# Optimization experiments

Measured on AMD Instinct MI355X. Metric: run time of the kernel, lower is better.

## Reference

```python
import jax, jax.numpy as jnp
import numpy as np

NUM_HEADS = 16
DIM = 1024
HEAD_DIM = DIM // NUM_HEADS
SCALE = HEAD_DIM ** -0.5


def setup_inputs() -> dict:
    key = jax.random.key(0)
    ks = jax.random.split(key, 6)
    b, n = 2, 1024
    x = jax.random.normal(ks[0], (b, n, DIM), dtype=jnp.float32)
    Wq = jax.random.normal(ks[1], (DIM, DIM), dtype=jnp.float32) * 0.02
    bq = jnp.zeros((DIM,), dtype=jnp.float32)
    Wkv = jax.random.normal(ks[2], (2 * DIM, DIM), dtype=jnp.float32) * 0.02
    bkv = jnp.zeros((2 * DIM,), dtype=jnp.float32)
    Wp = jax.random.normal(ks[3], (DIM, DIM), dtype=jnp.float32) * 0.02
    bp = jnp.zeros((DIM,), dtype=jnp.float32)
    return {"x": x, "Wq": Wq, "bq": bq, "Wkv": Wkv, "bkv": bkv, "Wp": Wp, "bp": bp}


def reference(x, Wq, bq, Wkv, bkv, Wp, bp):
    b, n, c = x.shape
    h, dh = NUM_HEADS, HEAD_DIM
    # self-attention: y = x
    q = (x @ Wq.T + bq).reshape(b, n, h, dh)              # bnhd
    kv = (x @ Wkv.T + bkv).reshape(b, n, 2, h, dh)
    k, v = kv[:, :, 0], kv[:, :, 1]                       # bmhd each
    attn = jnp.einsum('bnhd,bmhd->bnmh', q, k) * SCALE    # bnmh scores
    attn = jax.nn.softmax(attn, axis=2)                   # softmax over m
    out = jnp.einsum('bnmh,bmhd->bnhd', attn, v).reshape(b, n, c)
    out = out @ Wp.T + bp
    return (out, attn)
```

## Files before the change

### kernel.cpp

```cpp
#include <hip/hip_runtime.h>
#include <hip/hip_bf16.h>
#include <stdint.h>


#define NB   2
#define SEQ  1024
#define CDIM 1024
#define NH   16
#define HD   64
#define ROWS (NB*SEQ)
#define ATT_SCALE 0.125f
#define S23  1028

typedef __attribute__((ext_vector_type(8))) short bf16x8;
typedef __attribute__((ext_vector_type(4))) float f32x4;

#define MFMA16(a,b,c) __builtin_amdgcn_mfma_f32_16x16x32_bf16((a),(b),(c),0,0,0)

static __device__ __forceinline__ unsigned short f2bf(float f) {
  uint32_t x = __builtin_bit_cast(uint32_t, f);
  return (unsigned short)((x + 0x7fffu + ((x >> 16) & 1u)) >> 16);
}
static __device__ __forceinline__ float bf2f(unsigned short u) {
  uint32_t x = ((uint32_t)u) << 16;
  return __builtin_bit_cast(float, x);
}

static __device__ __forceinline__ void gl_lds16(const unsigned short* g,
                                                unsigned short* l) {
  __builtin_amdgcn_global_load_lds(
      (const __attribute__((address_space(1))) unsigned int*)g,
      (__attribute__((address_space(3))) unsigned int*)l,
      16, 0, 0);
}

__global__ __launch_bounds__(256) void k_convert(
    const float* __restrict__ x, const float* __restrict__ Wq,
    const float* __restrict__ Wkv, const float* __restrict__ Wp,
    unsigned short* __restrict__ Xhi, unsigned short* __restrict__ Xlo,
    unsigned short* __restrict__ Whi, unsigned short* __restrict__ Wlo)
{
  const int NX = ROWS * CDIM;
  const int NW = 4096 * CDIM;
  int i = blockIdx.x * 256 + threadIdx.x;
  if (i < NX) {
    float f = x[i];
    unsigned short h = f2bf(f);
    Xhi[i] = h; Xlo[i] = f2bf(f - bf2f(h));
  } else if (i < NX + NW) {
    int w = i - NX;
    int j = w >> 10, c = w & 1023;
    float f = (j < 1024) ? Wq[(size_t)j*1024 + c]
            : (j < 3072) ? Wkv[(size_t)(j-1024)*1024 + c]
                         : Wp[(size_t)(j-3072)*1024 + c];
    unsigned short h = f2bf(f);
    Whi[w] = h; Wlo[w] = f2bf(f - bf2f(h));
  }
}

struct EpiQKV {
  const float* bq; const float* bkv;
  unsigned short *Qhi, *Qlo, *Khi, *Klo, *Vthi, *Vtlo;
  __device__ __forceinline__ void operator()(int m, int n, float v) const {
    if (n < 1024) {
      v += bq[n];
      unsigned short h = f2bf(v);
      size_t o = (size_t)m*1024 + n;
      Qhi[o] = h; Qlo[o] = f2bf(v - bf2f(h));
    } else if (n < 2048) {
      v += bkv[n - 1024];
      size_t o = (size_t)m*1024 + (n - 1024);
      unsigned short h = f2bf(v);
      Khi[o] = h; Klo[o] = f2bf(v - bf2f(h));
    } else {
      v += bkv[n - 1024];
      int c = n - 2048;
      int hh = c >> 6, d = c & 63;
      int b = m >> 10, mm = m & 1023;
      size_t o = ((size_t)((b*NH + hh)*HD + d))*SEQ + mm;
      unsigned short h = f2bf(v);
      Vthi[o] = h; Vtlo[o] = f2bf(v - bf2f(h));
    }
  }
};
struct EpiOut {
  const float* bp; float* out;
  __device__ __forceinline__ void operator()(int m, int n, float v) const {
    out[(size_t)m*1024 + n] = v + bp[n];
  }
};

template <int BM, int BN, class Epi>
__device__ __forceinline__ void gemm_core(
    const unsigned short* __restrict__ Ahi, const unsigned short* __restrict__ Alo, int lda,
    const unsigned short* __restrict__ Bhi, const unsigned short* __restrict__ Blo, int ldb,
    int K, const Epi& epi)
{
  constexpr int FM = BM/32, FN = BN/32;
  constexpr int CA = BM/16, CB = BN/16;
  constexpr int TOT = 2*(CA+CB);
  __shared__ unsigned short sAh[BM*32], sAl[BM*32], sBh[BN*32], sBl[BN*32];
  const int tid  = threadIdx.x;
  const int lane = tid & 63, wave = tid >> 6;
  const int wm = wave & 1, wn = wave >> 1;
  const int bn = blockIdx.x * BN, bm = blockIdx.y * BM;
  const int r = lane & 15, q = lane >> 4;
  const int crow = lane >> 2, ccol = (lane & 3) * 8;

  f32x4 acc[FM][FN];
  #pragma unroll
  for (int i = 0; i < FM; i++)
    #pragma unroll
    for (int j = 0; j < FN; j++) {
      acc[i][j][0]=0.f; acc[i][j][1]=0.f; acc[i][j][2]=0.f; acc[i][j][3]=0.f;
    }

  for (int k0 = 0; k0 < K; k0 += 32) {
    #pragma unroll
    for (int t = 0; t < TOT/4; t++) {
      int c = wave + t*4;
      const unsigned short* gb; unsigned short* sb; int rr, grow, ld;
      if (c < CA)            { gb=Ahi; sb=sAh; rr=c;         grow=bm; ld=lda; }
      else if (c < 2*CA)     { gb=Alo; sb=sAl; rr=c-CA;      grow=bm; ld=lda; }
      else if (c < 2*CA+CB)  { gb=Bhi; sb=sBh; rr=c-2*CA;    grow=bn; ld=ldb; }
      else                   { gb=Blo; sb=sBl; rr=c-2*CA-CB; grow=bn; ld=ldb; }
      int row = rr*16 + crow;
      gl_lds16(gb + (size_t)(grow + row)*ld + k0 + ccol, sb + rr*512);
    }
    __syncthreads();
    bf16x8 ah[FM], al[FM], bh[FN], bl[FN];
    #pragma unroll
    for (int i = 0; i < FM; i++) {
      int oa = (wm*(BM/2) + i*16 + r)*32 + q*8;
      ah[i] = *(const bf16x8*)(sAh + oa);
      al[i] = *(const bf16x8*)(sAl + oa);
    }
    #pragma unroll
    for (int j = 0; j < FN; j++) {
      int ob = (wn*(BN/2) + j*16 + r)*32 + q*8;
      bh[j] = *(const bf16x8*)(sBh + ob);
      bl[j] = *(const bf16x8*)(sBl + ob);
    }
    #pragma unroll
    for (int i = 0; i < FM; i++)
      #pragma unroll
      for (int j = 0; j < FN; j++) {
        acc[i][j] = MFMA16(ah[i], bh[j], acc[i][j]);
        acc[i][j] = MFMA16(ah[i], bl[j], acc[i][j]);
        acc[i][j] = MFMA16(al[i], bh[j], acc[i][j]);
      }
    __syncthreads();
  }
  #pragma unroll
  for (int i = 0; i < FM; i++)
    #pragma unroll
    for (int j = 0; j < FN; j++)
      #pragma unroll
      for (int t = 0; t < 4; t++)
        epi(bm + wm*(BM/2) + i*16 + q*4 + t, bn + wn*(BN/2) + j*16 + r, acc[i][j][t]);
}

__global__ __launch_bounds__(256) void k_gemm_qkv(
    const unsigned short* Xhi, const unsigned short* Xlo,
    const unsigned short* Whi, const unsigned short* Wlo,
    const float* bq, const float* bkv,
    unsigned short* Qhi, unsigned short* Qlo,
    unsigned short* Khi, unsigned short* Klo,
    unsigned short* Vthi, unsigned short* Vtlo)
{
  EpiQKV e{bq, bkv, Qhi, Qlo, Khi, Klo, Vthi, Vtlo};
  gemm_core<128,128>(Xhi, Xlo, CDIM, Whi, Wlo, CDIM, CDIM, e);
}

__global__ __launch_bounds__(256) void k_gemm_out(
    const unsigned short* OAhi, const unsigned short* OAlo,
    const unsigned short* Wphi, const unsigned short* Wplo,
    const float* bp, float* out)
{
  EpiOut e{bp, out};
  gemm_core<64,64>(OAhi, OAlo, CDIM, Wphi, Wplo, CDIM, CDIM, e);
}

static __device__ __forceinline__ void stage_q23(
    const unsigned short* Qhi, const unsigned short* Qlo,
    size_t qrow0, int col0, unsigned short* sQ,
    int wave, int drow, int dseg)
{
  if (wave < 4) {
    int p = wave >> 1, t = wave & 1;
    const unsigned short* g = p ? Qlo : Qhi;
    gl_lds16(g + (qrow0 + t*8 + drow)*CDIM + col0 + dseg*8,
             sQ + p*1024 + t*512);
  }
}
static __device__ __forceinline__ void stage_k23(
    const unsigned short* Khi, const unsigned short* Klo,
    size_t krow0, int col0, unsigned short* dstbuf,
    int wave, int drow, int dseg)
{
  #pragma unroll
  for (int u = 0; u < 4; u++) {
    int c = wave*4 + u;
    int p = c >> 4, t = c & 15;
    const unsigned short* g = p ? Klo : Khi;
    gl_lds16(g + (krow0 + t*8 + drow)*CDIM + col0 + dseg*8,
             dstbuf + p*8192 + t*512);
  }
}

__global__ __launch_bounds__(512) void k_logits_softmax(
    const unsigned short* __restrict__ Qhi, const unsigned short* __restrict__ Qlo,
    const unsigned short* __restrict__ Khi, const unsigned short* __restrict__ Klo,
    unsigned short* __restrict__ P)
{
  const int nt = blockIdx.x, hg = blockIdx.y, b = blockIdx.z;
  const int n0 = nt*16;
  __shared__ unsigned short sQ[2*1024];
  __shared__ unsigned short sK[2][2*8192];
  __shared__ float slab[16*S23];
  __shared__ float red[512];
  __shared__ float gmax[16], gscale[16];
  const int tid = threadIdx.x, lane = tid & 63, wave = tid >> 6;
  const int r = lane & 15, q = lane >> 4;
  const int drow = lane >> 3, dseg = (lane & 7) ^ drow;
  const int sw = r & 7;
  const size_t qrow0 = (size_t)b*SEQ + n0;
  const size_t krow0 = (size_t)b*SEQ;

  {
    int col0 = (hg*8)*HD;
    stage_q23(Qhi, Qlo, qrow0, col0, sQ, wave, drow, dseg);
    stage_k23(Khi, Klo, krow0, col0, sK[0], wave, drow, dseg);
  }

  for (int hh = 0; hh < 8; hh++) {
    const int h = hg*8 + hh;
    const int col0 = h*HD;
    __syncthreads();
    bf16x8 qh[2], ql[2];
    #pragma unroll
    for (int ks = 0; ks < 2; ks++) {
      int phys = r*64 + (((ks*4 + q) ^ sw))*8;
      qh[ks] = *(const bf16x8*)(sQ + phys);
      ql[ks] = *(const bf16x8*)(sQ + 1024 + phys);
    }
    for (int c128 = 0; c128 < 8; c128++) {
      unsigned short* cur = sK[c128 & 1];
      if (c128 < 7)
        stage_k23(Khi, Klo, krow0 + (size_t)(c128+1)*128, col0,
                  sK[(c128+1)&1], wave, drow, dseg);
      {
        const int mb = wave*16;
        f32x4 acc; acc[0]=0.f; acc[1]=0.f; acc[2]=0.f; acc[3]=0.f;
        #pragma unroll
        for (int ks = 0; ks < 2; ks++) {
          int phys = (mb + r)*64 + (((ks*4 + q) ^ sw))*8;
          bf16x8 kh = *(const bf16x8*)(cur + phys);
          bf16x8 kl = *(const bf16x8*)(cur + 8192 + phys);
          acc = MFMA16(qh[ks], kh, acc);
          acc = MFMA16(qh[ks], kl, acc);
          acc = MFMA16(ql[ks], kh, acc);
        }
        #pragma unroll
        for (int t = 0; t < 4; t++)
          slab[(q*4+t)*S23 + c128*128 + mb + r] = acc[t] * ATT_SCALE;
      }
      __syncthreads();
    }
    if (hh < 7) {
      int ncol = (h+1)*HD;
      stage_q23(Qhi, Qlo, qrow0, ncol, sQ, wave, drow, dseg);
      stage_k23(Khi, Klo, krow0, ncol, sK[0], wave, drow, dseg);
    }
    const int n = tid >> 5, c = tid & 31;
    float mx = -1e30f;
    #pragma unroll 8
    for (int j = 0; j < 32; j++)
      mx = fmaxf(mx, slab[n*S23 + c + j*32]);
    red[tid] = mx;
    __syncthreads();
    if (tid < 16) {
      float m2 = red[tid*32];
      for (int j = 1; j < 32; j++) m2 = fmaxf(m2, red[tid*32 + j]);
      gmax[tid] = m2;
    }
    __syncthreads();
    const float gm = gmax[n];
    float s = 0.f;
    #pragma unroll 8
    for (int j = 0; j < 32; j++) {
      int idx = n*S23 + c + j*32;
      float p = __expf(slab[idx] - gm);
      slab[idx] = p;
      s += p;
    }
    red[tid] = s;
    __syncthreads();
    if (tid < 16) {
      float s2 = 0.f;
      for (int j = 0; j < 32; j++) s2 += red[tid*32 + j];
      gscale[tid] = 65535.0f / s2;
    }
    __syncthreads();
    const float sc = gscale[n];
    const size_t pb = ((size_t)((b*NH + h)*SEQ) + n0 + n)*SEQ;
    #pragma unroll
    for (int j = 0; j < 4; j++) {
      int m0 = (j*32 + c)*8;
      float4 v0 = *(const float4*)&slab[n*S23 + m0];
      float4 v1 = *(const float4*)&slab[n*S23 + m0 + 4];
      unsigned int u0 = (unsigned)(v0.x*sc + 0.5f) | ((unsigned)(v0.y*sc + 0.5f) << 16);
      unsigned int u1 = (unsigned)(v0.z*sc + 0.5f) | ((unsigned)(v0.w*sc + 0.5f) << 16);
      unsigned int u2 = (unsigned)(v1.x*sc + 0.5f) | ((unsigned)(v1.y*sc + 0.5f) << 16);
      unsigned int u3 = (unsigned)(v1.z*sc + 0.5f) | ((unsigned)(v1.w*sc + 0.5f) << 16);
      *(uint4*)(P + pb + m0) = make_uint4(u0, u1, u2, u3);
    }
  }
}

__global__ __launch_bounds__(256) void k_attn_write(
    const unsigned short* __restrict__ P, float* __restrict__ attn)
{
  int T = blockIdx.x*256 + threadIdx.x;
  int b = T >> 20, rem = T & 1048575;
  int n = rem >> 10, m = rem & 1023;
  const size_t pb = ((size_t)(b*NH)*SEQ + n)*SEQ + m;
  float v[16];
  #pragma unroll
  for (int h = 0; h < 16; h++)
    v[h] = (float)P[pb + (size_t)h*SEQ*SEQ] * (1.0f/65535.0f);
  size_t ob = ((size_t)(b*SEQ + n)*SEQ + m)*16;
  #pragma unroll
  for (int g = 0; g < 4; g++)
    *(float4*)(attn + ob + g*4) = make_float4(v[g*4], v[g*4+1], v[g*4+2], v[g*4+3]);
}

__global__ __launch_bounds__(256) void k_pv(
    const unsigned short* __restrict__ P,
    const unsigned short* __restrict__ Vthi, const unsigned short* __restrict__ Vtlo,
    unsigned short* __restrict__ OAhi, unsigned short* __restrict__ OAlo)
{
  int nt = blockIdx.x, h = blockIdx.y, b = blockIdx.z;
  int n0 = nt * 64;
  __shared__ unsigned short sPa[64*32], sPb[64*32], sVh[64*32], sVl[64*32];
  const int tid = threadIdx.x, lane = tid & 63, wave = tid >> 6;
  const int wm = wave & 1, wn = wave >> 1;
  const int r = lane & 15, q = lane >> 4;
  const int crow = lane >> 2, ccol = (lane & 3) * 8;
  const size_t pbase = ((size_t)(b*NH + h))*SEQ*SEQ;
  const size_t vbase = ((size_t)(b*NH + h))*HD*SEQ;

  f32x4 acc[2][2];
  #pragma unroll
  for (int i = 0; i < 2; i++)
    #pragma unroll
    for (int j = 0; j < 2; j++) {
      acc[i][j][0]=0.f; acc[i][j][1]=0.f; acc[i][j][2]=0.f; acc[i][j][3]=0.f;
    }

  for (int k0 = 0; k0 < SEQ; k0 += 32) {
    #pragma unroll
    for (int t = 0; t < 2; t++) {
      int c = wave + t*4;
      const unsigned short* gb = (c < 4) ? Vthi : Vtlo;
      unsigned short* sb = (c < 4) ? (unsigned short*)sVh : (unsigned short*)sVl;
      int rr = c & 3;
      int row = rr*16 + crow;
      gl_lds16(gb + vbase + (size_t)row*SEQ + k0 + ccol, sb + rr*512);
    }
    {
      int row = tid >> 2, ch = (tid & 3) * 8;
      uint4 v = *(const uint4*)(P + pbase + (size_t)(n0 + row)*SEQ + k0 + ch);
      unsigned int wds[4] = {v.x, v.y, v.z, v.w};
      unsigned int pa[4], pb4[4];
      #pragma unroll
      for (int e = 0; e < 4; e++) {
        unsigned int lo16 = wds[e] & 0xFFFFu;
        unsigned int hi16 = wds[e] >> 16;
        unsigned int a0 = __builtin_bit_cast(uint32_t, (float)(lo16 & 0xFF00u)) >> 16;
        unsigned int b0 = __builtin_bit_cast(uint32_t, (float)(lo16 & 0x00FFu)) >> 16;
        unsigned int a1 = __builtin_bit_cast(uint32_t, (float)(hi16 & 0xFF00u)) >> 16;
        unsigned int b1 = __builtin_bit_cast(uint32_t, (float)(hi16 & 0x00FFu)) >> 16;
        pa[e]  = a0 | (a1 << 16);
        pb4[e] = b0 | (b1 << 16);
      }
      *(uint4*)(sPa + row*32 + ch) = make_uint4(pa[0],pa[1],pa[2],pa[3]);
      *(uint4*)(sPb + row*32 + ch) = make_uint4(pb4[0],pb4[1],pb4[2],pb4[3]);
    }
    __syncthreads();
    bf16x8 pa[2], pb2[2], vh[2], vl[2];
    #pragma unroll
    for (int i = 0; i < 2; i++) {
      int off = (wm*32 + i*16 + r)*32 + q*8;
      pa[i]  = *(const bf16x8*)(sPa + off);
      pb2[i] = *(const bf16x8*)(sPb + off);
    }
    #pragma unroll
    for (int j = 0; j < 2; j++) {
      int off = (wn*32 + j*16 + r)*32 + q*8;
      vh[j] = *(const bf16x8*)(sVh + off);
      vl[j] = *(const bf16x8*)(sVl + off);
    }
    #pragma unroll
    for (int i = 0; i < 2; i++)
      #pragma unroll
      for (int j = 0; j < 2; j++) {
        acc[i][j] = MFMA16(pa[i],  vh[j], acc[i][j]);
        acc[i][j] = MFMA16(pb2[i], vh[j], acc[i][j]);
        acc[i][j] = MFMA16(pa[i],  vl[j], acc[i][j]);
      }
    __syncthreads();
  }
  #pragma unroll
  for (int i = 0; i < 2; i++)
    #pragma unroll
    for (int t = 0; t < 4; t++) {
      int nn = n0 + wm*32 + i*16 + q*4 + t;
      #pragma unroll
      for (int j = 0; j < 2; j++) {
        int d = wn*32 + j*16 + r;
        float val = acc[i][j][t] * (1.0f/65535.0f);
        size_t o = (size_t)(b*SEQ + nn)*CDIM + h*HD + d;
        unsigned short hb = f2bf(val);
        OAhi[o] = hb; OAlo[o] = f2bf(val - bf2f(hb));
      }
    }
}

extern "C" void kernel_launch(void* const* d_in, const int* in_sizes, int n_in,
                              void* d_out, int out_size, void* d_ws, size_t ws_size,
                              hipStream_t stream)
{
  const float* x   = (const float*)d_in[0];
  const float* Wq  = (const float*)d_in[1];
  const float* bq  = (const float*)d_in[2];
  const float* Wkv = (const float*)d_in[3];
  const float* bkv = (const float*)d_in[4];
  const float* Wp  = (const float*)d_in[5];
  const float* bp  = (const float*)d_in[6];

  float* out  = (float*)d_out;
  float* attn = out + (size_t)ROWS*CDIM;

  char* w = (char*)d_ws;
  unsigned short* Xhi  = (unsigned short*)w; w += (size_t)ROWS*CDIM*2;
  unsigned short* Xlo  = (unsigned short*)w; w += (size_t)ROWS*CDIM*2;
  unsigned short* Whi  = (unsigned short*)w; w += (size_t)4096*CDIM*2;
  unsigned short* Wlo  = (unsigned short*)w; w += (size_t)4096*CDIM*2;
  unsigned short* Qhi  = (unsigned short*)w; w += (size_t)ROWS*CDIM*2;
  unsigned short* Qlo  = (unsigned short*)w; w += (size_t)ROWS*CDIM*2;
  unsigned short* Khi  = (unsigned short*)w; w += (size_t)ROWS*CDIM*2;
  unsigned short* Klo  = (unsigned short*)w; w += (size_t)ROWS*CDIM*2;
  unsigned short* Vthi = (unsigned short*)w; w += (size_t)NB*NH*HD*SEQ*2;
  unsigned short* Vtlo = (unsigned short*)w; w += (size_t)NB*NH*HD*SEQ*2;
  unsigned short* OAhi = (unsigned short*)w; w += (size_t)ROWS*CDIM*2;
  unsigned short* OAlo = (unsigned short*)w; w += (size_t)ROWS*CDIM*2;
  unsigned short* P    = (unsigned short*)w; w += (size_t)NB*NH*SEQ*SEQ*2;

  k_convert<<<dim3((ROWS*CDIM + 4096*CDIM)/256), 256, 0, stream>>>(
      x, Wq, Wkv, Wp, Xhi, Xlo, Whi, Wlo);

  k_gemm_qkv<<<dim3(3072/128, 2048/128), 256, 0, stream>>>(
      Xhi, Xlo, Whi, Wlo, bq, bkv, Qhi, Qlo, Khi, Klo, Vthi, Vtlo);

  k_logits_softmax<<<dim3(SEQ/16, 2, NB), 512, 0, stream>>>(
      Qhi, Qlo, Khi, Klo, P);

  k_pv<<<dim3(SEQ/64, NH, NB), 256, 0, stream>>>(P, Vthi, Vtlo, OAhi, OAlo);

  k_gemm_out<<<dim3(1024/64, 2048/64), 256, 0, stream>>>(
      OAhi, OAlo, Whi + (size_t)3072*CDIM, Wlo + (size_t)3072*CDIM, bp, out);

  k_attn_write<<<dim3((NB*SEQ*SEQ)/256), 256, 0, stream>>>(P, attn);
}
```

Measured before the change: 410.0 us.

## Replace LDS softmax slab with two-pass online softmax recomputing logits

The logits/softmax kernel no longer keeps a 16x1024 fp32 score slab in shared memory. It runs a first pass that computes QK^T with an online running max and sum in registers, then a second pass that recomputes the logits and writes normalized P directly. The attention scale moves into the Q projection epilogue, and the grid now covers one head and 32 query rows per block, so far less LDS is used and occupancy can rise. The cost is doing the QK MFMA work twice and reloading the K tiles.

```diff
diff --git a/kernel.cpp b/kernel.cpp
--- a/kernel.cpp
+++ b/kernel.cpp
@@ -10,7 +10,6 @@
 #define HD   64
 #define ROWS (NB*SEQ)
 #define ATT_SCALE 0.125f
-#define S23  1028
 
 typedef __attribute__((ext_vector_type(8))) short bf16x8;
 typedef __attribute__((ext_vector_type(4))) float f32x4;
@@ -63,7 +62,7 @@
   unsigned short *Qhi, *Qlo, *Khi, *Klo, *Vthi, *Vtlo;
   __device__ __forceinline__ void operator()(int m, int n, float v) const {
     if (n < 1024) {
-      v += bq[n];
+      v = (v + bq[n]) * ATT_SCALE;
       unsigned short h = f2bf(v);
       size_t o = (size_t)m*1024 + n;
       Qhi[o] = h; Qlo[o] = f2bf(v - bf2f(h));
@@ -181,45 +180,18 @@
   gemm_core<64,64>(OAhi, OAlo, CDIM, Wphi, Wplo, CDIM, CDIM, e);
 }
 
-static __device__ __forceinline__ void stage_q23(
-    const unsigned short* Qhi, const unsigned short* Qlo,
-    size_t qrow0, int col0, unsigned short* sQ,
-    int wave, int drow, int dseg)
-{
-  if (wave < 4) {
-    int p = wave >> 1, t = wave & 1;
-    const unsigned short* g = p ? Qlo : Qhi;
-    gl_lds16(g + (qrow0 + t*8 + drow)*CDIM + col0 + dseg*8,
-             sQ + p*1024 + t*512);
-  }
-}
-static __device__ __forceinline__ void stage_k23(
-    const unsigned short* Khi, const unsigned short* Klo,
-    size_t krow0, int col0, unsigned short* dstbuf,
-    int wave, int drow, int dseg)
-{
-  #pragma unroll
-  for (int u = 0; u < 4; u++) {
-    int c = wave*4 + u;
-    int p = c >> 4, t = c & 15;
-    const unsigned short* g = p ? Klo : Khi;
-    gl_lds16(g + (krow0 + t*8 + drow)*CDIM + col0 + dseg*8,
-             dstbuf + p*8192 + t*512);
-  }
-}
-
-__global__ __launch_bounds__(512) void k_logits_softmax(
+__global__ __launch_bounds__(512, 4) void k_logits_softmax(
     const unsigned short* __restrict__ Qhi, const unsigned short* __restrict__ Qlo,
     const unsigned short* __restrict__ Khi, const unsigned short* __restrict__ Klo,
     unsigned short* __restrict__ P)
 {
-  const int nt = blockIdx.x, hg = blockIdx.y, b = blockIdx.z;
-  const int n0 = nt*16;
-  __shared__ unsigned short sQ[2*1024];
-  __shared__ unsigned short sK[2][2*8192];
-  __shared__ float slab[16*S23];
-  __shared__ float red[512];
-  __shared__ float gmax[16], gscale[16];
+  const int nt = blockIdx.x, h = blockIdx.y, b = blockIdx.z;
+  const int n0 = nt*32;
+  const int col0 = h*HD;
+  __shared__ unsigned short sQ[2*32*64];
+  __shared__ unsigned short sK[2][2*128*64];
+  __shared__ float redm[8][32], reds[8][32];
+  __shared__ float gm_s[32], sc_s[32];
   const int tid = threadIdx.x, lane = tid & 63, wave = tid >> 6;
   const int r = lane & 15, q = lane >> 4;
   const int drow = lane >> 3, dseg = (lane & 7) ^ drow;
@@ -227,94 +199,126 @@
   const size_t qrow0 = (size_t)b*SEQ + n0;
   const size_t krow0 = (size_t)b*SEQ;
 
+  auto stageK = [&](int c, int buf) {
+    unsigned short* dst = sK[buf];
+    #pragma unroll
+    for (int u = 0; u < 4; u++) {
+      int cc = wave*4 + u;
+      int p = cc >> 4, t = cc & 15;
+      const unsigned short* g = p ? Klo : Khi;
+      gl_lds16(g + (krow0 + (size_t)c*128 + t*8 + drow)*CDIM + col0 + dseg*8,
+               dst + p*8192 + t*512);
+    }
+  };
+
   {
-    int col0 = (hg*8)*HD;
-    stage_q23(Qhi, Qlo, qrow0, col0, sQ, wave, drow, dseg);
-    stage_k23(Khi, Klo, krow0, col0, sK[0], wave, drow, dseg);
-  }
-
-  for (int hh = 0; hh < 8; hh++) {
-    const int h = hg*8 + hh;
-    const int col0 = h*HD;
-    __syncthreads();
-    bf16x8 qh[2], ql[2];
+    int p = wave >> 2, t = wave & 3;
+    const unsigned short* g = p ? Qlo : Qhi;
+    gl_lds16(g + (qrow0 + t*8 + drow)*CDIM + col0 + dseg*8,
+             sQ + p*2048 + t*512);
+    stageK(0, 0);
+  }
+  __syncthreads();
+
+  bf16x8 qh[2][2], ql[2][2];
+  #pragma unroll
+  for (int nf = 0; nf < 2; nf++)
     #pragma unroll
     for (int ks = 0; ks < 2; ks++) {
-      int phys = r*64 + (((ks*4 + q) ^ sw))*8;
-      qh[ks] = *(const bf16x8*)(sQ + phys);
-      ql[ks] = *(const bf16x8*)(sQ + 1024 + phys);
-    }
-    for (int c128 = 0; c128 < 8; c128++) {
-      unsigned short* cur = sK[c128 & 1];
-      if (c128 < 7)
-        stage_k23(Khi, Klo, krow0 + (size_t)(c128+1)*128, col0,
-                  sK[(c128+1)&1], wave, drow, dseg);
-      {
-        const int mb = wave*16;
-        f32x4 acc; acc[0]=0.f; acc[1]=0.f; acc[2]=0.f; acc[3]=0.f;
-        #pragma unroll
-        for (int ks = 0; ks < 2; ks++) {
-          int phys = (mb + r)*64 + (((ks*4 + q) ^ sw))*8;
-          bf16x8 kh = *(const bf16x8*)(cur + phys);
-          bf16x8 kl = *(const bf16x8*)(cur + 8192 + phys);
-          acc = MFMA16(qh[ks], kh, acc);
-          acc = MFMA16(qh[ks], kl, acc);
-          acc = MFMA16(ql[ks], kh, acc);
-        }
-        #pragma unroll
-        for (int t = 0; t < 4; t++)
-          slab[(q*4+t)*S23 + c128*128 + mb + r] = acc[t] * ATT_SCALE;
-      }
-      __syncthreads();
-    }
-    if (hh < 7) {
-      int ncol = (h+1)*HD;
-      stage_q23(Qhi, Qlo, qrow0, ncol, sQ, wave, drow, dseg);
-      stage_k23(Khi, Klo, krow0, ncol, sK[0], wave, drow, dseg);
-    }
-    const int n = tid >> 5, c = tid & 31;
-    float mx = -1e30f;
-    #pragma unroll 8
-    for (int j = 0; j < 32; j++)
-      mx = fmaxf(mx, slab[n*S23 + c + j*32]);
-    red[tid] = mx;
-    __syncthreads();
-    if (tid < 16) {
-      float m2 = red[tid*32];
-      for (int j = 1; j < 32; j++) m2 = fmaxf(m2, red[tid*32 + j]);
-      gmax[tid] = m2;
-    }
-    __syncthreads();
-    const float gm = gmax[n];
-    float s = 0.f;
-    #pragma unroll 8
-    for (int j = 0; j < 32; j++) {
-      int idx = n*S23 + c + j*32;
-      float p = __expf(slab[idx] - gm);
-      slab[idx] = p;
-      s += p;
-    }
-    red[tid] = s;
-    __syncthreads();
-    if (tid < 16) {
-      float s2 = 0.f;
-      for (int j = 0; j < 32; j++) s2 += red[tid*32 + j];
-      gscale[tid] = 65535.0f / s2;
-    }
-    __syncthreads();
-    const float sc = gscale[n];
-    const size_t pb = ((size_t)((b*NH + h)*SEQ) + n0 + n)*SEQ;
-    #pragma unroll
-    for (int j = 0; j < 4; j++) {
-      int m0 = (j*32 + c)*8;
-      float4 v0 = *(const float4*)&slab[n*S23 + m0];
-      float4 v1 = *(const float4*)&slab[n*S23 + m0 + 4];
-      unsigned int u0 = (unsigned)(v0.x*sc + 0.5f) | ((unsigned)(v0.y*sc + 0.5f) << 16);
-      unsigned int u1 = (unsigned)(v0.z*sc + 0.5f) | ((unsigned)(v0.w*sc + 0.5f) << 16);
-      unsigned int u2 = (unsigned)(v1.x*sc + 0.5f) | ((unsigned)(v1.y*sc + 0.5f) << 16);
-      unsigned int u3 = (unsigned)(v1.z*sc + 0.5f) | ((unsigned)(v1.w*sc + 0.5f) << 16);
-      *(uint4*)(P + pb + m0) = make_uint4(u0, u1, u2, u3);
-    }
+      int phys = (nf*16 + r)*64 + (((ks*4 + q) ^ sw))*8;
+      qh[nf][ks] = *(const bf16x8*)(sQ + phys);
+      ql[nf][ks] = *(const bf16x8*)(sQ + 2048 + phys);
+    }
+
+  const int mb = wave*16;
+
+  float mx[2] = {-1e30f, -1e30f}, sm[2] = {0.f, 0.f};
+  for (int c = 0; c < 8; c++) {
+    if (c < 7) stageK(c+1, (c+1)&1);
+    const unsigned short* cur = sK[c&1];
+    bf16x8 kh[2], kl[2];
+    #pragma unroll
+    for (int ks = 0; ks < 2; ks++) {
+      int phys = (mb + r)*64 + (((ks*4 + q) ^ sw))*8;
+      kh[ks] = *(const bf16x8*)(cur + phys);
+      kl[ks] = *(const bf16x8*)(cur + 8192 + phys);
+    }
+    #pragma unroll
+    for (int nf = 0; nf < 2; nf++) {
+      f32x4 acc; acc[0]=0.f; acc[1]=0.f; acc[2]=0.f; acc[3]=0.f;
+      #pragma unroll
+      for (int ks = 0; ks < 2; ks++) {
+        acc = MFMA16(kh[ks], qh[nf][ks], acc);
+        acc = MFMA16(kl[ks], qh[nf][ks], acc);
+        acc = MFMA16(kh[ks], ql[nf][ks], acc);
+      }
+      float vmax = fmaxf(fmaxf(acc[0], acc[1]), fmaxf(acc[2], acc[3]));
+      float mnew = fmaxf(mx[nf], vmax);
+      sm[nf] = sm[nf]*__expf(mx[nf]-mnew)
+             + __expf(acc[0]-mnew) + __expf(acc[1]-mnew)
+             + __expf(acc[2]-mnew) + __expf(acc[3]-mnew);
+      mx[nf] = mnew;
+    }
+    __syncthreads();
+  }
+
+  #pragma unroll
+  for (int nf = 0; nf < 2; nf++) {
+    #pragma unroll
+    for (int off = 16; off <= 32; off <<= 1) {
+      float mo = __shfl_xor(mx[nf], off);
+      float so = __shfl_xor(sm[nf], off);
+      float mn = fmaxf(mx[nf], mo);
+      sm[nf] = sm[nf]*__expf(mx[nf]-mn) + so*__expf(mo-mn);
+      mx[nf] = mn;
+    }
+  }
+  if (q < 2) { redm[wave][q*16 + r] = mx[q]; reds[wave][q*16 + r] = sm[q]; }
+  stageK(0, 0);
+  __syncthreads();
+  if (tid < 32) {
+    float m2 = redm[0][tid], s2 = reds[0][tid];
+    #pragma unroll
+    for (int w2 = 1; w2 < 8; w2++) {
+      float mo = redm[w2][tid], so = reds[w2][tid];
+      float mn = fmaxf(m2, mo);
+      s2 = s2*__expf(m2-mn) + so*__expf(mo-mn);
+      m2 = mn;
+    }
+    gm_s[tid] = m2; sc_s[tid] = 65535.0f / s2;
+  }
+  __syncthreads();
+  const float gm[2] = {gm_s[r], gm_s[16 + r]};
+  const float sc[2] = {sc_s[r], sc_s[16 + r]};
+
+  const size_t pbase = ((size_t)(b*NH + h)*SEQ + n0)*SEQ;
+  for (int c = 0; c < 8; c++) {
+    if (c < 7) stageK(c+1, (c+1)&1);
+    const unsigned short* cur = sK[c&1];
+    bf16x8 kh[2], kl[2];
+    #pragma unroll
+    for (int ks = 0; ks < 2; ks++) {
+      int phys = (mb + r)*64 + (((ks*4 + q) ^ sw))*8;
+      kh[ks] = *(const bf16x8*)(cur + phys);
+      kl[ks] = *(const bf16x8*)(cur + 8192 + phys);
+    }
+    #pragma unroll
+    for (int nf = 0; nf < 2; nf++) {
+      f32x4 acc; acc[0]=0.f; acc[1]=0.f; acc[2]=0.f; acc[3]=0.f;
+      #pragma unroll
+      for (int ks = 0; ks < 2; ks++) {
+        acc = MFMA16(kh[ks], qh[nf][ks], acc);
+        acc = MFMA16(kl[ks], qh[nf][ks], acc);
+        acc = MFMA16(kh[ks], ql[nf][ks], acc);
+      }
+      unsigned int u0 = (unsigned)(__expf(acc[0]-gm[nf])*sc[nf] + 0.5f)
+                      | ((unsigned)(__expf(acc[1]-gm[nf])*sc[nf] + 0.5f) << 16);
+      unsigned int u1 = (unsigned)(__expf(acc[2]-gm[nf])*sc[nf] + 0.5f)
+                      | ((unsigned)(__expf(acc[3]-gm[nf])*sc[nf] + 0.5f) << 16);
+      *(uint2*)(P + pbase + (size_t)(nf*16 + r)*SEQ + c*128 + mb + q*4) =
+          make_uint2(u0, u1);
+    }
+    __syncthreads();
   }
 }
 
@@ -463,7 +467,7 @@
   k_gemm_qkv<<<dim3(3072/128, 2048/128), 256, 0, stream>>>(
       Xhi, Xlo, Whi, Wlo, bq, bkv, Qhi, Qlo, Khi, Klo, Vthi, Vtlo);
 
-  k_logits_softmax<<<dim3(SEQ/16, 2, NB), 512, 0, stream>>>(
+  k_logits_softmax<<<dim3(SEQ/32, NH, NB), 512, 0, stream>>>(
       Qhi, Qlo, Khi, Klo, P);
 
   k_pv<<<dim3(SEQ/64, NH, NB), 256, 0, stream>>>(P, Vthi, Vtlo, OAhi, OAlo);
```

Measured after the change: 394.5 us. -3.8%, faster.
